# Kernel tuning notes

Measured on AMD Instinct MI355X. Metric: run time of the kernel, lower is better.

The kernel has to match this reference:

```python
import jax, jax.numpy as jnp
import numpy as np

N_NODES = 50000


def _add_self_loops(edge_index, num_nodes):
    loop = jnp.arange(num_nodes, dtype=edge_index.dtype)
    row = jnp.concatenate([edge_index[0], loop])
    col = jnp.concatenate([edge_index[1], loop])
    return row, col


def _gcn_norm(row, col, num_nodes):
    # deg computed on target index with unit edge weights (PyG gcn_norm)
    deg = jax.ops.segment_sum(jnp.ones_like(col, dtype=jnp.float32), col,
                              num_segments=num_nodes)
    dis = jnp.where(deg > 0, jax.lax.rsqrt(jnp.maximum(deg, 1.0)), 0.0)
    return dis[row] * dis[col]  # [E]


def _gcn_conv(x, W, b, row, col, norm, num_nodes):
    h = x @ W                                  # dense transform first (PyG order)
    msg = h[row] * norm[:, None]               # gather + normalize
    out = jax.ops.segment_sum(msg, col, num_segments=num_nodes)  # scatter-add
    return out + b


def setup_inputs() -> dict:
    key = jax.random.key(0)
    ks = jax.random.split(key, 10)
    E = 800000
    x = jax.random.normal(ks[0], (N_NODES, 29), dtype=jnp.float32)
    edge_index = jax.random.randint(ks[1], (2, E), 0, N_NODES, dtype=jnp.int64)

    def glorot(k, fan_in, fan_out):
        s = jnp.sqrt(2.0 / (fan_in + fan_out)).astype(jnp.float32)
        return jax.random.normal(k, (fan_in, fan_out), dtype=jnp.float32) * s

    return {
        "x": x, "edge_index": edge_index,
        "W1": glorot(ks[2], 29, 96),  "b1": jnp.zeros((96,), jnp.float32),
        "W2": glorot(ks[3], 96, 128), "b2": jnp.zeros((128,), jnp.float32),
        "W3": glorot(ks[4], 128, 64), "b3": jnp.zeros((64,), jnp.float32),
        "W4": glorot(ks[5], 64, 32),  "b4": jnp.zeros((32,), jnp.float32),
    }


def reference(x, edge_index, W1, b1, W2, b2, W3, b3, W4, b4):
    row, col = _add_self_loops(edge_index, N_NODES)
    norm = _gcn_norm(row, col, N_NODES)  # same graph -> same norm for all layers
    h = _gcn_conv(x, W1, b1, row, col, norm, N_NODES)
    h = jax.nn.relu(h)
    # dropout(p=0.4) is identity in eval mode
    h = _gcn_conv(h, W2, b2, row, col, norm, N_NODES)
    h = _gcn_conv(h, W3, b3, row, col, norm, N_NODES)
    h = _gcn_conv(h, W4, b4, row, col, norm, N_NODES)
    return h
```

## Files before the change

### kernel.cpp

```cpp
#include <hip/hip_runtime.h>
#include <hip/hip_fp16.h>


constexpr int NN  = 50000;
constexpr int CAP = 64;
constexpr int AGB = (NN * 8 + 255) / 256;
constexpr int C1B = (NN + 255) / 256;
constexpr int PREPB = (NN * 32 + 64 + 255) / 256;
constexpr int W34XB = 17;
constexpr int W234XB = 13;
constexpr int PXB = 256;

typedef unsigned short u16;
typedef int iv4 __attribute__((ext_vector_type(4)));

__device__ __forceinline__ float4 h4_to_f4(uint2 q) {
    union { unsigned u; __half2 h; } a, b;
    a.u = q.x; b.u = q.y;
    const float2 lo = __half22float2(a.h);
    const float2 hi = __half22float2(b.h);
    return make_float4(lo.x, lo.y, hi.x, hi.y);
}
__device__ __forceinline__ uint2 f4_to_h4(float4 v) {
    union { unsigned u; __half2 h; } a, b;
    a.h = __float22half2_rn(make_float2(v.x, v.y));
    b.h = __float22half2_rn(make_float2(v.z, v.w));
    return make_uint2(a.u, b.u);
}

__global__ void place_x_kernel(const int* __restrict__ row, const int* __restrict__ col,
                               int* __restrict__ cnt, u16* __restrict__ ell, int E) {
    const int g  = blockIdx.x & 7;
    const int bi = blockIdx.x >> 3;
    const int n4 = E >> 2;
    const int slice = (n4 + PXB - 1) / PXB;
    const int i0 = bi * slice;
    int i1 = i0 + slice; if (i1 > n4) i1 = n4;
    const iv4* cv = (const iv4*)col;
    const iv4* rv = (const iv4*)row;
#define PLACE1(cc, rr) {                                                        \
        const int c_ = (cc);                                                    \
        if ((((c_ >> 6) & 7) == g) && (unsigned)c_ < (unsigned)NN) {            \
            const int r_ = (rr);                                                \
            if ((unsigned)r_ < (unsigned)NN) {                                  \
                const int pos = atomicAdd(&cnt[c_], 1);                         \
                if (pos < CAP) ell[c_ * CAP + pos] = (u16)r_;                   \
            }                                                                   \
        }                                                                       \
    }
    for (int i = i0 + threadIdx.x; i < i1; i += 256) {
        const iv4 c4 = cv[i];
        const iv4 r4 = rv[i];
        PLACE1(c4.x, r4.x);
        PLACE1(c4.y, r4.y);
        PLACE1(c4.z, r4.z);
        PLACE1(c4.w, r4.w);
    }
    if (bi == 0) {
        for (int e = (n4 << 2) + threadIdx.x; e < E; e += 256) {
            const int c = col[e];
            if (((c >> 6) & 7) != g || (unsigned)c >= (unsigned)NN) continue;
            const int r = row[e];
            if ((unsigned)r >= (unsigned)NN) continue;
            const int pos = atomicAdd(&cnt[c], 1);
            if (pos < CAP) ell[c * CAP + pos] = (u16)r;
        }
    }
#undef PLACE1
}

__global__ void prep_all_kernel(const int* __restrict__ cnt, u16* __restrict__ ell,
                                const float* __restrict__ x, float* __restrict__ dis,
                                float* __restrict__ Ba, float* __restrict__ Bb,
                                unsigned* __restrict__ Ha, unsigned* __restrict__ Hb,
                                float* __restrict__ c1d,
                                const float* __restrict__ W3, const float* __restrict__ W4,
                                const float* __restrict__ b3,
                                float* __restrict__ W34, float* __restrict__ v1) {
    if (blockIdx.x >= PREPB) {
        const int wid = (blockIdx.x - PREPB) * 256 + threadIdx.x;
        if (wid < 4096) {
            const int r = wid >> 5, j = wid & 31;
            float a = 0.f;
#pragma unroll 8
            for (int k = 0; k < 64; ++k) a = fmaf(W3[r * 64 + k], W4[k * 32 + j], a);
            W34[wid] = a;
        } else if (wid < 4128) {
            const int j = wid - 4096;
            float a = 0.f;
#pragma unroll 8
            for (int k = 0; k < 64; ++k) a = fmaf(b3[k], W4[k * 32 + j], a);
            v1[j] = a;
        }
        return;
    }
    const int idx = blockIdx.x * blockDim.x + threadIdx.x;
    if (idx < NN * 32) {
        const int n = idx >> 5, f = idx & 31;
        int m = cnt[n]; if (m > CAP) m = CAP;
        const float d = rsqrtf((float)m + 1.0f);
        Ba[idx] = (f < 29) ? x[n * 29 + f] * d : 0.f;
        if (f == 31) dis[n] = d;
        if (f == 30) {
            int mp = (m + 7) & ~7; if (mp > CAP) mp = CAP;
            for (int k = m; k < mp; ++k) ell[n * CAP + k] = (u16)NN;
        }
    } else {
        const int i = idx - NN * 32;
        if (i < 32) { Ba[NN * 32 + i] = 0.f; Bb[NN * 32 + i] = 0.f; }
        if (i < 16) { Ha[NN * 16 + i] = 0u; Hb[NN * 16 + i] = 0u; }
        if (i == 32) dis[NN] = 0.f;
        else if (i == 33) c1d[NN] = 0.f;
    }
}

__device__ __forceinline__ void agg32_body(const float* __restrict__ hs,
                                           const int* __restrict__ cnt,
                                           const u16* __restrict__ ell,
                                           const float* __restrict__ dis,
                                           float* __restrict__ out) {
    const int idx = blockIdx.x * blockDim.x + threadIdx.x;
    if (idx >= NN * 8) return;
    const int n = idx >> 3, c = idx & 7;
    const float4* hpc = (const float4*)hs + c;
    float4 acc = hpc[n * 8];
    int m = cnt[n]; if (m > CAP) m = CAP;
    const int m8 = (m + 7) >> 3;
    const int4* ip = (const int4*)(ell + (size_t)n * CAP);
    int t = 0;
    for (; t + 2 <= m8; t += 2) {
        const int4 sA = ip[t], sB = ip[t + 1];
        const unsigned ax = (unsigned)sA.x, ay = (unsigned)sA.y;
        const unsigned az = (unsigned)sA.z, aw = (unsigned)sA.w;
        const unsigned bx = (unsigned)sB.x, by = (unsigned)sB.y;
        const unsigned bz = (unsigned)sB.z, bw = (unsigned)sB.w;
        const float4 g0 = hpc[(ax & 0xFFFFu) * 8], g1 = hpc[(ax >> 16) * 8];
        const float4 g2 = hpc[(ay & 0xFFFFu) * 8], g3 = hpc[(ay >> 16) * 8];
        const float4 g4 = hpc[(az & 0xFFFFu) * 8], g5 = hpc[(az >> 16) * 8];
        const float4 g6 = hpc[(aw & 0xFFFFu) * 8], g7 = hpc[(aw >> 16) * 8];
        const float4 h0 = hpc[(bx & 0xFFFFu) * 8], h1 = hpc[(bx >> 16) * 8];
        const float4 h2 = hpc[(by & 0xFFFFu) * 8], h3 = hpc[(by >> 16) * 8];
        const float4 h4 = hpc[(bz & 0xFFFFu) * 8], h5 = hpc[(bz >> 16) * 8];
        const float4 h6 = hpc[(bw & 0xFFFFu) * 8], h7 = hpc[(bw >> 16) * 8];
        acc.x += (((g0.x + g1.x) + (g2.x + g3.x)) + ((g4.x + g5.x) + (g6.x + g7.x)))
               + (((h0.x + h1.x) + (h2.x + h3.x)) + ((h4.x + h5.x) + (h6.x + h7.x)));
        acc.y += (((g0.y + g1.y) + (g2.y + g3.y)) + ((g4.y + g5.y) + (g6.y + g7.y)))
               + (((h0.y + h1.y) + (h2.y + h3.y)) + ((h4.y + h5.y) + (h6.y + h7.y)));
        acc.z += (((g0.z + g1.z) + (g2.z + g3.z)) + ((g4.z + g5.z) + (g6.z + g7.z)))
               + (((h0.z + h1.z) + (h2.z + h3.z)) + ((h4.z + h5.z) + (h6.z + h7.z)));
        acc.w += (((g0.w + g1.w) + (g2.w + g3.w)) + ((g4.w + g5.w) + (g6.w + g7.w)))
               + (((h0.w + h1.w) + (h2.w + h3.w)) + ((h4.w + h5.w) + (h6.w + h7.w)));
    }
    if (t < m8) {
        const int4 s = ip[t];
        const unsigned ux = (unsigned)s.x, uy = (unsigned)s.y;
        const unsigned uz = (unsigned)s.z, uw = (unsigned)s.w;
        const float4 g0 = hpc[(ux & 0xFFFFu) * 8], g1 = hpc[(ux >> 16) * 8];
        const float4 g2 = hpc[(uy & 0xFFFFu) * 8], g3 = hpc[(uy >> 16) * 8];
        const float4 g4 = hpc[(uz & 0xFFFFu) * 8], g5 = hpc[(uz >> 16) * 8];
        const float4 g6 = hpc[(uw & 0xFFFFu) * 8], g7 = hpc[(uw >> 16) * 8];
        acc.x += ((g0.x + g1.x) + (g2.x + g3.x)) + ((g4.x + g5.x) + (g6.x + g7.x));
        acc.y += ((g0.y + g1.y) + (g2.y + g3.y)) + ((g4.y + g5.y) + (g6.y + g7.y));
        acc.z += ((g0.z + g1.z) + (g2.z + g3.z)) + ((g4.z + g5.z) + (g6.z + g7.z));
        acc.w += ((g0.w + g1.w) + (g2.w + g3.w)) + ((g4.w + g5.w) + (g6.w + g7.w));
    }
    const float d = dis[n];
    float4 r;
    r.x = acc.x * d; r.y = acc.y * d; r.z = acc.z * d; r.w = acc.w * d;
    ((float4*)out)[idx] = r;
}

template<int MODE>
__device__ __forceinline__ void agg32h_body(const uint2* __restrict__ hh,
                                            const int* __restrict__ cnt,
                                            const u16* __restrict__ ell,
                                            const float* __restrict__ dis,
                                            const float* __restrict__ c1,
                                            const float* __restrict__ c2,
                                            const float* __restrict__ v1,
                                            const float* __restrict__ v2,
                                            const float* __restrict__ bv,
                                            void* __restrict__ out) {
    const int idx = blockIdx.x * blockDim.x + threadIdx.x;
    if (idx >= NN * 8) return;
    const int n = idx >> 3, c = idx & 7;
    const uint2* hpc = hh + c;
    float4 acc = h4_to_f4(hpc[(size_t)n * 8]);
    int m = cnt[n]; if (m > CAP) m = CAP;
    const int m8 = (m + 7) >> 3;
    const int4* ip = (const int4*)(ell + (size_t)n * CAP);
    int t = 0;
    for (; t + 2 <= m8; t += 2) {
        const int4 sA = ip[t], sB = ip[t + 1];
        const unsigned ax = (unsigned)sA.x, ay = (unsigned)sA.y;
        const unsigned az = (unsigned)sA.z, aw = (unsigned)sA.w;
        const unsigned bx = (unsigned)sB.x, by = (unsigned)sB.y;
        const unsigned bz = (unsigned)sB.z, bw = (unsigned)sB.w;
        const uint2 q0 = hpc[(ax & 0xFFFFu) * 8], q1 = hpc[(ax >> 16) * 8];
        const uint2 q2 = hpc[(ay & 0xFFFFu) * 8], q3 = hpc[(ay >> 16) * 8];
        const uint2 q4 = hpc[(az & 0xFFFFu) * 8], q5 = hpc[(az >> 16) * 8];
        const uint2 q6 = hpc[(aw & 0xFFFFu) * 8], q7 = hpc[(aw >> 16) * 8];
        const uint2 q8 = hpc[(bx & 0xFFFFu) * 8], q9 = hpc[(bx >> 16) * 8];
        const uint2 qa = hpc[(by & 0xFFFFu) * 8], qb = hpc[(by >> 16) * 8];
        const uint2 qc = hpc[(bz & 0xFFFFu) * 8], qd = hpc[(bz >> 16) * 8];
        const uint2 qe = hpc[(bw & 0xFFFFu) * 8], qf = hpc[(bw >> 16) * 8];
        const float4 g0 = h4_to_f4(q0), g1 = h4_to_f4(q1);
        const float4 g2 = h4_to_f4(q2), g3 = h4_to_f4(q3);
        const float4 g4 = h4_to_f4(q4), g5 = h4_to_f4(q5);
        const float4 g6 = h4_to_f4(q6), g7 = h4_to_f4(q7);
        const float4 h0 = h4_to_f4(q8), h1 = h4_to_f4(q9);
        const float4 h2 = h4_to_f4(qa), h3 = h4_to_f4(qb);
        const float4 h4 = h4_to_f4(qc), h5 = h4_to_f4(qd);
        const float4 h6 = h4_to_f4(qe), h7 = h4_to_f4(qf);
        acc.x += (((g0.x + g1.x) + (g2.x + g3.x)) + ((g4.x + g5.x) + (g6.x + g7.x)))
               + (((h0.x + h1.x) + (h2.x + h3.x)) + ((h4.x + h5.x) + (h6.x + h7.x)));
        acc.y += (((g0.y + g1.y) + (g2.y + g3.y)) + ((g4.y + g5.y) + (g6.y + g7.y)))
               + (((h0.y + h1.y) + (h2.y + h3.y)) + ((h4.y + h5.y) + (h6.y + h7.y)));
        acc.z += (((g0.z + g1.z) + (g2.z + g3.z)) + ((g4.z + g5.z) + (g6.z + g7.z)))
               + (((h0.z + h1.z) + (h2.z + h3.z)) + ((h4.z + h5.z) + (h6.z + h7.z)));
        acc.w += (((g0.w + g1.w) + (g2.w + g3.w)) + ((g4.w + g5.w) + (g6.w + g7.w)))
               + (((h0.w + h1.w) + (h2.w + h3.w)) + ((h4.w + h5.w) + (h6.w + h7.w)));
    }
    if (t < m8) {
        const int4 s = ip[t];
        const unsigned ux = (unsigned)s.x, uy = (unsigned)s.y;
        const unsigned uz = (unsigned)s.z, uw = (unsigned)s.w;
        const uint2 q0 = hpc[(ux & 0xFFFFu) * 8], q1 = hpc[(ux >> 16) * 8];
        const uint2 q2 = hpc[(uy & 0xFFFFu) * 8], q3 = hpc[(uy >> 16) * 8];
        const uint2 q4 = hpc[(uz & 0xFFFFu) * 8], q5 = hpc[(uz >> 16) * 8];
        const uint2 q6 = hpc[(uw & 0xFFFFu) * 8], q7 = hpc[(uw >> 16) * 8];
        const float4 g0 = h4_to_f4(q0), g1 = h4_to_f4(q1);
        const float4 g2 = h4_to_f4(q2), g3 = h4_to_f4(q3);
        const float4 g4 = h4_to_f4(q4), g5 = h4_to_f4(q5);
        const float4 g6 = h4_to_f4(q6), g7 = h4_to_f4(q7);
        acc.x += ((g0.x + g1.x) + (g2.x + g3.x)) + ((g4.x + g5.x) + (g6.x + g7.x));
        acc.y += ((g0.y + g1.y) + (g2.y + g3.y)) + ((g4.y + g5.y) + (g6.y + g7.y));
        acc.z += ((g0.z + g1.z) + (g2.z + g3.z)) + ((g4.z + g5.z) + (g6.z + g7.z));
        acc.w += ((g0.w + g1.w) + (g2.w + g3.w)) + ((g4.w + g5.w) + (g6.w + g7.w));
    }
    const float d = dis[n];
    if (MODE == 1) {
        const float d2 = d * d;
        float4 r;
        r.x = acc.x * d2; r.y = acc.y * d2; r.z = acc.z * d2; r.w = acc.w * d2;
        ((uint2*)out)[(size_t)n * 8 + c] = f4_to_h4(r);
    } else {
        const float a1 = c1[n], a2 = c2[n];
        const float4 w1 = ((const float4*)v1)[c];
        const float4 w2 = ((const float4*)v2)[c];
        const float4 bb = ((const float4*)bv)[c];
        float4 r;
        r.x = fmaf(acc.x, d, fmaf(a1, w1.x, fmaf(a2, w2.x, bb.x)));
        r.y = fmaf(acc.y, d, fmaf(a1, w1.y, fmaf(a2, w2.y, bb.y)));
        r.z = fmaf(acc.z, d, fmaf(a1, w1.z, fmaf(a2, w2.z, bb.z)));
        r.w = fmaf(acc.w, d, fmaf(a1, w1.w, fmaf(a2, w2.w, bb.w)));
        ((float4*)out)[idx] = r;
    }
}

__device__ __forceinline__ void agg1_body(const float* __restrict__ in,
                                          const int* __restrict__ cnt,
                                          const u16* __restrict__ ell,
                                          const float* __restrict__ dis,
                                          float* __restrict__ out,
                                          float* __restrict__ outd, int blk0) {
    const int n = (blockIdx.x - blk0) * 256 + threadIdx.x;
    if (n >= NN) return;
    float acc = in[n];
    int m = cnt[n]; if (m > CAP) m = CAP;
    const int m8 = (m + 7) >> 3;
    const iv4* ip = (const iv4*)(ell + (size_t)n * CAP);
    for (int t = 0; t < m8; ++t) {
        const iv4 s = ip[t];
        const unsigned ux = (unsigned)s.x, uy = (unsigned)s.y;
        const unsigned uz = (unsigned)s.z, uw = (unsigned)s.w;
        acc += ((in[ux & 0xFFFFu] + in[ux >> 16]) + (in[uy & 0xFFFFu] + in[uy >> 16]))
             + ((in[uz & 0xFFFFu] + in[uz >> 16]) + (in[uw & 0xFFFFu] + in[uw >> 16]));
    }
    const float r = dis[n] * acc;
    out[n] = r;
    if (outd) outd[n] = r * dis[n];
}

__global__ void agg_pre_kernel(const float* __restrict__ Ba, const int* __restrict__ cnt,
                               const u16* __restrict__ ell, const float* __restrict__ dis,
                               float* __restrict__ Bb, float* __restrict__ c1,
                               float* __restrict__ c1d,
                               const float* __restrict__ W2, const float* __restrict__ b2,
                               const float* __restrict__ W34, float* __restrict__ W234,
                               float* __restrict__ v2) {
    if (blockIdx.x < AGB) {
        agg32_body(Ba, cnt, ell, dis, Bb);
    } else if (blockIdx.x < AGB + C1B) {
        agg1_body(dis, cnt, ell, dis, c1, c1d, AGB);
    } else {
        const int wid = (blockIdx.x - AGB - C1B) * 256 + threadIdx.x;
        if (wid < 3072) {
            const int r = wid >> 5, j = wid & 31;
            float a = 0.f;
#pragma unroll 8
            for (int k = 0; k < 128; ++k) a = fmaf(W2[r * 128 + k], W34[k * 32 + j], a);
            W234[wid] = a;
        } else if (wid < 3104) {
            const int j = wid - 3072;
            float a = 0.f;
#pragma unroll 8
            for (int k = 0; k < 128; ++k) a = fmaf(b2[k], W34[k * 32 + j], a);
            v2[j] = a;
        }
    }
}

__global__ void agg_hop1_kernel(const uint2* __restrict__ Ha, const int* __restrict__ cnt,
                                const u16* __restrict__ ell, const float* __restrict__ dis,
                                uint2* __restrict__ Hb, const float* __restrict__ c1d,
                                float* __restrict__ c2) {
    if (blockIdx.x < AGB)
        agg32h_body<1>(Ha, cnt, ell, dis, nullptr, nullptr, nullptr, nullptr, nullptr, Hb);
    else
        agg1_body(c1d, cnt, ell, dis, c2, nullptr, AGB);
}

__global__ void agg_hop2_kernel(const uint2* __restrict__ Hb, const int* __restrict__ cnt,
                                const u16* __restrict__ ell, const float* __restrict__ dis,
                                uint2* __restrict__ Ha) {
    agg32h_body<1>(Hb, cnt, ell, dis, nullptr, nullptr, nullptr, nullptr, nullptr, Ha);
}

__global__ void agg_hop3_kernel(const uint2* __restrict__ Ha, const int* __restrict__ cnt,
                                const u16* __restrict__ ell, const float* __restrict__ dis,
                                const float* __restrict__ c1, const float* __restrict__ c2,
                                const float* __restrict__ v1, const float* __restrict__ v2,
                                const float* __restrict__ bv, float* __restrict__ out) {
    agg32h_body<2>(Ha, cnt, ell, dis, c1, c2, v1, v2, bv, out);
}

__global__ void __launch_bounds__(192, 2)
gemm_fused_kernel(const float* __restrict__ X, const float* __restrict__ W1,
                  const float* __restrict__ b1, const float* __restrict__ dis,
                  const float* __restrict__ W234, uint2* __restrict__ G) {
    constexpr int NPB = 16, RSX = 36, RSH = 104;
    __shared__ float xs[NPB * RSX];
    __shared__ float hsm[NPB * RSH];
    const int tid = threadIdx.x;
    const int n0  = blockIdx.x * NPB;

    const float4* Xv = (const float4*)(X + (size_t)n0 * 32);
    for (int i = tid; i < NPB * 8; i += 192) {
        const int nl = i >> 3, r = i & 7;
        float4 v = make_float4(0.f, 0.f, 0.f, 0.f);
        if (n0 + nl < NN) v = Xv[nl * 8 + r];
        *(float4*)(xs + nl * RSX + r * 4) = v;
    }
    __syncthreads();

    {
        const int cg = tid % 24, g = tid / 24;
        const float* x0 = xs + (2 * g) * RSX;
        const float* x1 = x0 + RSX;
        const float4* Wv = (const float4*)W1;
        float4 a0 = make_float4(0.f, 0.f, 0.f, 0.f);
        float4 a1 = make_float4(0.f, 0.f, 0.f, 0.f);
#pragma unroll
        for (int k = 0; k < 29; ++k) {
            const float4 w = Wv[k * 24 + cg];
            const float v0 = x0[k], v1 = x1[k];
            a0.x = fmaf(v0, w.x, a0.x); a0.y = fmaf(v0, w.y, a0.y);
            a0.z = fmaf(v0, w.z, a0.z); a0.w = fmaf(v0, w.w, a0.w);
            a1.x = fmaf(v1, w.x, a1.x); a1.y = fmaf(v1, w.y, a1.y);
            a1.z = fmaf(v1, w.z, a1.z); a1.w = fmaf(v1, w.w, a1.w);
        }
        const float4 bb = ((const float4*)b1)[cg];
#pragma unroll
        for (int h = 0; h < 2; ++h) {
            const int nl = 2 * g + h, node = n0 + nl;
            const float d = (node < NN) ? dis[node] : 0.f;
            const float4 a = h ? a1 : a0;
            float4 r;
            r.x = fmaxf(a.x + bb.x, 0.f) * d; r.y = fmaxf(a.y + bb.y, 0.f) * d;
            r.z = fmaxf(a.z + bb.z, 0.f) * d; r.w = fmaxf(a.w + bb.w, 0.f) * d;
            *(float4*)(hsm + nl * RSH + cg * 4) = r;
        }
    }
    __syncthreads();

    if (tid < 128) {
        const int nl = tid >> 3, cg = tid & 7;
        const float* hr = hsm + nl * RSH;
        const float4* Wv = (const float4*)W234;
        float4 a = make_float4(0.f, 0.f, 0.f, 0.f);
#pragma unroll 8
        for (int k = 0; k < 96; ++k) {
            const float4 w = Wv[k * 8 + cg];
            const float v = hr[k];
            a.x = fmaf(v, w.x, a.x); a.y = fmaf(v, w.y, a.y);
            a.z = fmaf(v, w.z, a.z); a.w = fmaf(v, w.w, a.w);
        }
        const int node = n0 + nl;
        if (node < NN) G[(size_t)node * 8 + cg] = f4_to_h4(a);
    }
}

extern "C" void kernel_launch(void* const* d_in, const int* in_sizes, int n_in,
                              void* d_out, int out_size, void* d_ws, size_t ws_size,
                              hipStream_t stream) {
    const float* x  = (const float*)d_in[0];
    const int*   ei = (const int*)d_in[1];
    const float* W1 = (const float*)d_in[2]; const float* b1 = (const float*)d_in[3];
    const float* W2 = (const float*)d_in[4]; const float* b2 = (const float*)d_in[5];
    const float* W3 = (const float*)d_in[6]; const float* b3 = (const float*)d_in[7];
    const float* W4 = (const float*)d_in[8]; const float* b4p = (const float*)d_in[9];
    float* outp = (float*)d_out;

    const int E = in_sizes[1] / 2;
    const int* row = ei;
    const int* col = ei + E;

    int*   cnt  = (int*)d_ws;
    float* dis  = (float*)(cnt + 50048);
    u16*   ell  = (u16*)(dis + 50064);
    float* c1   = (float*)((int*)ell + 1600000);
    float* c1d  = c1 + 50064;
    float* c2   = c1d + 50064;
    float* W34  = c2 + 50064;
    float* W234 = W34 + 4096;
    float* v1   = W234 + 3072;
    float* v2   = v1 + 32;
    float* Ba   = v2 + 32;
    float* Bb   = Ba + 1600064;
    unsigned* Ha = (unsigned*)(Bb + 1600064);
    unsigned* Hb = Ha + 800032;

    hipMemsetAsync(cnt, 0, 50048 * sizeof(int), stream);
    place_x_kernel<<<8 * PXB, 256, 0, stream>>>(row, col, cnt, ell, E);
    prep_all_kernel<<<PREPB + W34XB, 256, 0, stream>>>(cnt, ell, x, dis, Ba, Bb,
                                                       Ha, Hb, c1d, W3, W4, b3, W34, v1);
    agg_pre_kernel<<<AGB + C1B + W234XB, 256, 0, stream>>>(Ba, cnt, ell, dis, Bb, c1, c1d,
                                                           W2, b2, W34, W234, v2);
    gemm_fused_kernel<<<(NN + 15) / 16, 192, 0, stream>>>(Bb, W1, b1, dis, W234,
                                                          (uint2*)Ha);
    agg_hop1_kernel<<<AGB + C1B, 256, 0, stream>>>((const uint2*)Ha, cnt, ell, dis,
                                                   (uint2*)Hb, c1d, c2);
    agg_hop2_kernel<<<AGB, 256, 0, stream>>>((const uint2*)Hb, cnt, ell, dis, (uint2*)Ha);
    agg_hop3_kernel<<<AGB, 256, 0, stream>>>((const uint2*)Ha, cnt, ell, dis,
                                             c1, c2, v1, v2, b4p, outp);
}
```

Measured before the change: 212.3 us.

## Split neighbor gathers across lane halves with 16-byte loads and shuffle reduce

Each node's 8 threads are reorganised into 4 feature-quarter lanes times 2 edge-halves. Each thread now gathers 16-byte uint4 chunks (8 halfs) for half of the neighbors instead of 8-byte chunks for all of them. Partial sums are combined with a cross-lane xor shuffle, and outputs are written as uint4 by the lower 4 lanes, or redistributed by shuffle for the final layer. The aim is fewer, wider gather transactions per edge, at the cost of extra shuffles, idle lanes on store, and more registers.

```diff
diff --git a/kernel.cpp b/kernel.cpp
--- a/kernel.cpp
+++ b/kernel.cpp
@@ -14,18 +14,22 @@
 typedef unsigned short u16;
 typedef int iv4 __attribute__((ext_vector_type(4)));
 
-__device__ __forceinline__ float4 h4_to_f4(uint2 q) {
-    union { unsigned u; __half2 h; } a, b;
-    a.u = q.x; b.u = q.y;
-    const float2 lo = __half22float2(a.h);
-    const float2 hi = __half22float2(b.h);
-    return make_float4(lo.x, lo.y, hi.x, hi.y);
-}
 __device__ __forceinline__ uint2 f4_to_h4(float4 v) {
     union { unsigned u; __half2 h; } a, b;
     a.h = __float22half2_rn(make_float2(v.x, v.y));
     b.h = __float22half2_rn(make_float2(v.z, v.w));
     return make_uint2(a.u, b.u);
+}
+__device__ __forceinline__ void h8_to_f8(uint4 g, float4& lo, float4& hi) {
+    union { unsigned u; __half2 h; } t;
+    float2 f;
+    t.u = g.x; f = __half22float2(t.h); lo.x = f.x; lo.y = f.y;
+    t.u = g.y; f = __half22float2(t.h); lo.z = f.x; lo.w = f.y;
+    t.u = g.z; f = __half22float2(t.h); hi.x = f.x; hi.y = f.y;
+    t.u = g.w; f = __half22float2(t.h); hi.z = f.x; hi.w = f.y;
+}
+__device__ __forceinline__ float4 f4add(float4 a, float4 b) {
+    return make_float4(a.x + b.x, a.y + b.y, a.z + b.z, a.w + b.w);
 }
 
 __global__ void place_x_kernel(const int* __restrict__ row, const int* __restrict__ col,
@@ -171,7 +175,7 @@
 }
 
 template<int MODE>
-__device__ __forceinline__ void agg32h_body(const uint2* __restrict__ hh,
+__device__ __forceinline__ void agg32h_body(const uint4* __restrict__ hh,
                                             const int* __restrict__ cnt,
                                             const u16* __restrict__ ell,
                                             const float* __restrict__ dis,
@@ -184,67 +188,88 @@
     const int idx = blockIdx.x * blockDim.x + threadIdx.x;
     if (idx >= NN * 8) return;
     const int n = idx >> 3, c = idx & 7;
-    const uint2* hpc = hh + c;
-    float4 acc = h4_to_f4(hpc[(size_t)n * 8]);
+    const int q = c & 3;
+    const int h = c >> 2;
+    const uint4* hp = hh + q;
+    float4 aL, aH;
+    {
+        float4 sl, sh;
+        h8_to_f8(hp[(size_t)n * 4], sl, sh);
+        const float m0 = h ? 0.f : 1.f;
+        aL = make_float4(sl.x * m0, sl.y * m0, sl.z * m0, sl.w * m0);
+        aH = make_float4(sh.x * m0, sh.y * m0, sh.z * m0, sh.w * m0);
+    }
     int m = cnt[n]; if (m > CAP) m = CAP;
     const int m8 = (m + 7) >> 3;
     const int4* ip = (const int4*)(ell + (size_t)n * CAP);
     int t = 0;
     for (; t + 2 <= m8; t += 2) {
         const int4 sA = ip[t], sB = ip[t + 1];
-        const unsigned ax = (unsigned)sA.x, ay = (unsigned)sA.y;
-        const unsigned az = (unsigned)sA.z, aw = (unsigned)sA.w;
-        const unsigned bx = (unsigned)sB.x, by = (unsigned)sB.y;
-        const unsigned bz = (unsigned)sB.z, bw = (unsigned)sB.w;
-        const uint2 q0 = hpc[(ax & 0xFFFFu) * 8], q1 = hpc[(ax >> 16) * 8];
-        const uint2 q2 = hpc[(ay & 0xFFFFu) * 8], q3 = hpc[(ay >> 16) * 8];
-        const uint2 q4 = hpc[(az & 0xFFFFu) * 8], q5 = hpc[(az >> 16) * 8];
-        const uint2 q6 = hpc[(aw & 0xFFFFu) * 8], q7 = hpc[(aw >> 16) * 8];
-        const uint2 q8 = hpc[(bx & 0xFFFFu) * 8], q9 = hpc[(bx >> 16) * 8];
-        const uint2 qa = hpc[(by & 0xFFFFu) * 8], qb = hpc[(by >> 16) * 8];
-        const uint2 qc = hpc[(bz & 0xFFFFu) * 8], qd = hpc[(bz >> 16) * 8];
-        const uint2 qe = hpc[(bw & 0xFFFFu) * 8], qf = hpc[(bw >> 16) * 8];
-        const float4 g0 = h4_to_f4(q0), g1 = h4_to_f4(q1);
-        const float4 g2 = h4_to_f4(q2), g3 = h4_to_f4(q3);
-        const float4 g4 = h4_to_f4(q4), g5 = h4_to_f4(q5);
-        const float4 g6 = h4_to_f4(q6), g7 = h4_to_f4(q7);
-        const float4 h0 = h4_to_f4(q8), h1 = h4_to_f4(q9);
-        const float4 h2 = h4_to_f4(qa), h3 = h4_to_f4(qb);
-        const float4 h4 = h4_to_f4(qc), h5 = h4_to_f4(qd);
-        const float4 h6 = h4_to_f4(qe), h7 = h4_to_f4(qf);
-        acc.x += (((g0.x + g1.x) + (g2.x + g3.x)) + ((g4.x + g5.x) + (g6.x + g7.x)))
-               + (((h0.x + h1.x) + (h2.x + h3.x)) + ((h4.x + h5.x) + (h6.x + h7.x)));
-        acc.y += (((g0.y + g1.y) + (g2.y + g3.y)) + ((g4.y + g5.y) + (g6.y + g7.y)))
-               + (((h0.y + h1.y) + (h2.y + h3.y)) + ((h4.y + h5.y) + (h6.y + h7.y)));
-        acc.z += (((g0.z + g1.z) + (g2.z + g3.z)) + ((g4.z + g5.z) + (g6.z + g7.z)))
-               + (((h0.z + h1.z) + (h2.z + h3.z)) + ((h4.z + h5.z) + (h6.z + h7.z)));
-        acc.w += (((g0.w + g1.w) + (g2.w + g3.w)) + ((g4.w + g5.w) + (g6.w + g7.w)))
-               + (((h0.w + h1.w) + (h2.w + h3.w)) + ((h4.w + h5.w) + (h6.w + h7.w)));
+        const unsigned a0 = (unsigned)sA.x, a1 = (unsigned)sA.y;
+        const unsigned a2 = (unsigned)sA.z, a3 = (unsigned)sA.w;
+        const unsigned b0 = (unsigned)sB.x, b1 = (unsigned)sB.y;
+        const unsigned b2 = (unsigned)sB.z, b3 = (unsigned)sB.w;
+        const unsigned i0 = h ? (a0 >> 16) : (a0 & 0xFFFFu);
+        const unsigned i1 = h ? (a1 >> 16) : (a1 & 0xFFFFu);
+        const unsigned i2 = h ? (a2 >> 16) : (a2 & 0xFFFFu);
+        const unsigned i3 = h ? (a3 >> 16) : (a3 & 0xFFFFu);
+        const unsigned i4 = h ? (b0 >> 16) : (b0 & 0xFFFFu);
+        const unsigned i5 = h ? (b1 >> 16) : (b1 & 0xFFFFu);
+        const unsigned i6 = h ? (b2 >> 16) : (b2 & 0xFFFFu);
+        const unsigned i7 = h ? (b3 >> 16) : (b3 & 0xFFFFu);
+        const uint4 g0 = hp[(size_t)i0 * 4], g1 = hp[(size_t)i1 * 4];
+        const uint4 g2 = hp[(size_t)i2 * 4], g3 = hp[(size_t)i3 * 4];
+        const uint4 g4 = hp[(size_t)i4 * 4], g5 = hp[(size_t)i5 * 4];
+        const uint4 g6 = hp[(size_t)i6 * 4], g7 = hp[(size_t)i7 * 4];
+        float4 l0, h0, l1, h1, l2, h2, l3, h3, l4, h4, l5, h5, l6, h6, l7, h7;
+        h8_to_f8(g0, l0, h0); h8_to_f8(g1, l1, h1);
+        h8_to_f8(g2, l2, h2); h8_to_f8(g3, l3, h3);
+        h8_to_f8(g4, l4, h4); h8_to_f8(g5, l5, h5);
+        h8_to_f8(g6, l6, h6); h8_to_f8(g7, l7, h7);
+        aL = f4add(aL, f4add(f4add(f4add(l0, l1), f4add(l2, l3)),
+                             f4add(f4add(l4, l5), f4add(l6, l7))));
+        aH = f4add(aH, f4add(f4add(f4add(h0, h1), f4add(h2, h3)),
+                             f4add(f4add(h4, h5), f4add(h6, h7))));
     }
     if (t < m8) {
         const int4 s = ip[t];
-        const unsigned ux = (unsigned)s.x, uy = (unsigned)s.y;
-        const unsigned uz = (unsigned)s.z, uw = (unsigned)s.w;
-        const uint2 q0 = hpc[(ux & 0xFFFFu) * 8], q1 = hpc[(ux >> 16) * 8];
-        const uint2 q2 = hpc[(uy & 0xFFFFu) * 8], q3 = hpc[(uy >> 16) * 8];
-        const uint2 q4 = hpc[(uz & 0xFFFFu) * 8], q5 = hpc[(uz >> 16) * 8];
-        const uint2 q6 = hpc[(uw & 0xFFFFu) * 8], q7 = hpc[(uw >> 16) * 8];
-        const float4 g0 = h4_to_f4(q0), g1 = h4_to_f4(q1);
-        const float4 g2 = h4_to_f4(q2), g3 = h4_to_f4(q3);
-        const float4 g4 = h4_to_f4(q4), g5 = h4_to_f4(q5);
-        const float4 g6 = h4_to_f4(q6), g7 = h4_to_f4(q7);
-        acc.x += ((g0.x + g1.x) + (g2.x + g3.x)) + ((g4.x + g5.x) + (g6.x + g7.x));
-        acc.y += ((g0.y + g1.y) + (g2.y + g3.y)) + ((g4.y + g5.y) + (g6.y + g7.y));
-        acc.z += ((g0.z + g1.z) + (g2.z + g3.z)) + ((g4.z + g5.z) + (g6.z + g7.z));
-        acc.w += ((g0.w + g1.w) + (g2.w + g3.w)) + ((g4.w + g5.w) + (g6.w + g7.w));
-    }
+        const unsigned w0 = (unsigned)s.x, w1 = (unsigned)s.y;
+        const unsigned w2 = (unsigned)s.z, w3 = (unsigned)s.w;
+        const unsigned i0 = h ? (w0 >> 16) : (w0 & 0xFFFFu);
+        const unsigned i1 = h ? (w1 >> 16) : (w1 & 0xFFFFu);
+        const unsigned i2 = h ? (w2 >> 16) : (w2 & 0xFFFFu);
+        const unsigned i3 = h ? (w3 >> 16) : (w3 & 0xFFFFu);
+        const uint4 g0 = hp[(size_t)i0 * 4], g1 = hp[(size_t)i1 * 4];
+        const uint4 g2 = hp[(size_t)i2 * 4], g3 = hp[(size_t)i3 * 4];
+        float4 l0, h0, l1, h1, l2, h2, l3, h3;
+        h8_to_f8(g0, l0, h0); h8_to_f8(g1, l1, h1);
+        h8_to_f8(g2, l2, h2); h8_to_f8(g3, l3, h3);
+        aL = f4add(aL, f4add(f4add(l0, l1), f4add(l2, l3)));
+        aH = f4add(aH, f4add(f4add(h0, h1), f4add(h2, h3)));
+    }
+    aL.x += __shfl_xor(aL.x, 4); aL.y += __shfl_xor(aL.y, 4);
+    aL.z += __shfl_xor(aL.z, 4); aL.w += __shfl_xor(aL.w, 4);
+    aH.x += __shfl_xor(aH.x, 4); aH.y += __shfl_xor(aH.y, 4);
+    aH.z += __shfl_xor(aH.z, 4); aH.w += __shfl_xor(aH.w, 4);
     const float d = dis[n];
     if (MODE == 1) {
-        const float d2 = d * d;
-        float4 r;
-        r.x = acc.x * d2; r.y = acc.y * d2; r.z = acc.z * d2; r.w = acc.w * d2;
-        ((uint2*)out)[(size_t)n * 8 + c] = f4_to_h4(r);
+        if (c < 4) {
+            const float d2 = d * d;
+            float4 rl = make_float4(aL.x * d2, aL.y * d2, aL.z * d2, aL.w * d2);
+            float4 rh = make_float4(aH.x * d2, aH.y * d2, aH.z * d2, aH.w * d2);
+            const uint2 pl = f4_to_h4(rl), ph = f4_to_h4(rh);
+            uint4 o; o.x = pl.x; o.y = pl.y; o.z = ph.x; o.w = ph.y;
+            ((uint4*)out)[(size_t)n * 4 + q] = o;
+        }
     } else {
+        const int lane = threadIdx.x & 63;
+        const int src = (lane & ~7) | (c >> 1);
+        const float s0 = __shfl(aL.x, src), s1 = __shfl(aL.y, src);
+        const float s2 = __shfl(aL.z, src), s3 = __shfl(aL.w, src);
+        const float s4 = __shfl(aH.x, src), s5 = __shfl(aH.y, src);
+        const float s6 = __shfl(aH.z, src), s7 = __shfl(aH.w, src);
+        const float4 acc = (c & 1) ? make_float4(s4, s5, s6, s7)
+                                   : make_float4(s0, s1, s2, s3);
         const float a1 = c1[n], a2 = c2[n];
         const float4 w1 = ((const float4*)v1)[c];
         const float4 w2 = ((const float4*)v2)[c];
@@ -311,9 +336,9 @@
     }
 }
 
-__global__ void agg_hop1_kernel(const uint2* __restrict__ Ha, const int* __restrict__ cnt,
+__global__ void agg_hop1_kernel(const uint4* __restrict__ Ha, const int* __restrict__ cnt,
                                 const u16* __restrict__ ell, const float* __restrict__ dis,
-                                uint2* __restrict__ Hb, const float* __restrict__ c1d,
+                                uint4* __restrict__ Hb, const float* __restrict__ c1d,
                                 float* __restrict__ c2) {
     if (blockIdx.x < AGB)
         agg32h_body<1>(Ha, cnt, ell, dis, nullptr, nullptr, nullptr, nullptr, nullptr, Hb);
@@ -321,13 +346,13 @@
         agg1_body(c1d, cnt, ell, dis, c2, nullptr, AGB);
 }
 
-__global__ void agg_hop2_kernel(const uint2* __restrict__ Hb, const int* __restrict__ cnt,
+__global__ void agg_hop2_kernel(const uint4* __restrict__ Hb, const int* __restrict__ cnt,
                                 const u16* __restrict__ ell, const float* __restrict__ dis,
-                                uint2* __restrict__ Ha) {
+                                uint4* __restrict__ Ha) {
     agg32h_body<1>(Hb, cnt, ell, dis, nullptr, nullptr, nullptr, nullptr, nullptr, Ha);
 }
 
-__global__ void agg_hop3_kernel(const uint2* __restrict__ Ha, const int* __restrict__ cnt,
+__global__ void agg_hop3_kernel(const uint4* __restrict__ Ha, const int* __restrict__ cnt,
                                 const u16* __restrict__ ell, const float* __restrict__ dis,
                                 const float* __restrict__ c1, const float* __restrict__ c2,
                                 const float* __restrict__ v1, const float* __restrict__ v2,
@@ -439,9 +464,9 @@
                                                            W2, b2, W34, W234, v2);
     gemm_fused_kernel<<<(NN + 15) / 16, 192, 0, stream>>>(Bb, W1, b1, dis, W234,
                                                           (uint2*)Ha);
-    agg_hop1_kernel<<<AGB + C1B, 256, 0, stream>>>((const uint2*)Ha, cnt, ell, dis,
-                                                   (uint2*)Hb, c1d, c2);
-    agg_hop2_kernel<<<AGB, 256, 0, stream>>>((const uint2*)Hb, cnt, ell, dis, (uint2*)Ha);
-    agg_hop3_kernel<<<AGB, 256, 0, stream>>>((const uint2*)Ha, cnt, ell, dis,
+    agg_hop1_kernel<<<AGB + C1B, 256, 0, stream>>>((const uint4*)Ha, cnt, ell, dis,
+                                                   (uint4*)Hb, c1d, c2);
+    agg_hop2_kernel<<<AGB, 256, 0, stream>>>((const uint4*)Hb, cnt, ell, dis, (uint4*)Ha);
+    agg_hop3_kernel<<<AGB, 256, 0, stream>>>((const uint4*)Ha, cnt, ell, dis,
                                              c1, c2, v1, v2, b4p, outp);
 }
```

Measured after the change: 210.6 us. Within noise of the previous version (-0.8%).
